# Performance work log

Measured on AMD Instinct MI355X. Metric: run time of the kernel, lower is better.

Reference implementation:

```python
import jax, jax.numpy as jnp
import numpy as np

N = 50000          # total points
C = 256            # channels
H = 8              # heads
D = C // H         # head dim = 32
W = 256            # window size
STRIDE = 128
LENGTHS = [12500, 12500, 12500, 12500]
HID = 512          # ffn hidden = 2.0 * C
EPS = 1e-5


def _build_windows():
    """numpy port of build_windows_1d: returns (M, W) indices and bool mask."""
    idxs, masks = [], []
    start = 0
    for L in LENGTHS:
        n_windows = (L - 1) // STRIDE + 1
        for i in range(n_windows):
            s = i * STRIDE
            b = min(L, s + W)
            cur_len = b - s
            loc = np.arange(s, b, dtype=np.int32) + start
            if W - cur_len > 0:
                loc = np.concatenate([loc, np.full(W - cur_len, loc[-1], dtype=np.int32)])
            m = np.zeros(W, dtype=bool)
            m[:cur_len] = True
            idxs.append(loc)
            masks.append(m)
        start += L
    return np.stack(idxs, 0), np.stack(masks, 0)


def setup_inputs() -> dict:
    key = jax.random.key(0)
    ks = jax.random.split(key, 8)
    def p(k, shape):
        return jax.random.normal(k, shape, dtype=jnp.float32) * 0.02
    win_idx_np, win_mask_np = _build_windows()
    return {
        "x": jax.random.normal(ks[0], (N, C), dtype=jnp.float32),
        "win_idx": jnp.asarray(win_idx_np, dtype=jnp.int32),
        "win_mask": jnp.asarray(win_mask_np),
        "norm1_g": jnp.ones((C,), jnp.float32), "norm1_b": jnp.zeros((C,), jnp.float32),
        "qkv_w": p(ks[1], (C, 3 * C)),
        "proj_w": p(ks[2], (C, C)), "proj_b": jnp.zeros((C,), jnp.float32),
        "ca_norm_g": jnp.ones((C,), jnp.float32), "ca_norm_b": jnp.zeros((C,), jnp.float32),
        "ca_qkv_w": p(ks[3], (C, 3 * C)), "ca_qkv_b": jnp.zeros((3 * C,), jnp.float32),
        "ca_proj_w": p(ks[4], (C, C)), "ca_proj_b": jnp.zeros((C,), jnp.float32),
        "norm2_g": jnp.ones((C,), jnp.float32), "norm2_b": jnp.zeros((C,), jnp.float32),
        "ffn_w1": p(ks[5], (C, HID)), "ffn_b1": jnp.zeros((HID,), jnp.float32),
        "ffn_ln_g": jnp.ones((HID,), jnp.float32), "ffn_ln_b": jnp.zeros((HID,), jnp.float32),
        "ffn_w2": p(ks[6], (HID, C)), "ffn_b2": jnp.zeros((C,), jnp.float32),
    }


def _ln(x, g, b):
    m = jnp.mean(x, axis=-1, keepdims=True)
    v = jnp.mean((x - m) ** 2, axis=-1, keepdims=True)
    return (x - m) * jax.lax.rsqrt(v + EPS) * g + b


def reference(x, win_idx, win_mask,
              norm1_g, norm1_b, qkv_w, proj_w, proj_b,
              ca_norm_g, ca_norm_b, ca_qkv_w, ca_qkv_b, ca_proj_w, ca_proj_b,
              norm2_g, norm2_b, ffn_w1, ffn_b1, ffn_ln_g, ffn_ln_b, ffn_w2, ffn_b2):
    M, Wn = win_idx.shape
    scale = D ** -0.5
    maskf = win_mask[..., None].astype(x.dtype)          # [M, W, 1]

    x_in = _ln(x, norm1_g, norm1_b)                      # [N, C]
    xw = x_in[win_idx]                                   # gather windows [M, W, C]

    # --- Stream A: per-window SDPA ---
    qkv = xw @ qkv_w                                     # [M, W, 3C]
    q, k, v = [t.reshape(M, Wn, H, D).transpose(0, 2, 1, 3)
               for t in jnp.split(qkv, 3, axis=-1)]      # each [M, H, W, D]
    scores = jnp.einsum('mhqd,mhkd->mhqk', q, k) * scale
    scores = jnp.where(win_mask[:, None, None, :], scores, -jnp.inf)
    attn = jax.nn.softmax(scores, axis=-1)
    out = jnp.einsum('mhqk,mhkd->mhqd', attn, v).transpose(0, 2, 1, 3).reshape(M, Wn, C)
    out = (out @ proj_w + proj_b) * maskf                # masked per-window output

    # --- Stream B: centroid attention over M window centroids ---
    wc = jnp.maximum(win_mask.sum(-1, keepdims=True).astype(x.dtype), 1.0)  # [M, 1]
    cent = (xw * maskf).sum(1) / wc                      # [M, C]
    cx = _ln(cent, ca_norm_g, ca_norm_b)
    cqkv = cx @ ca_qkv_w + ca_qkv_b
    cq, ck, cv = [t.reshape(M, H, D).transpose(1, 0, 2)
                  for t in jnp.split(cqkv, 3, axis=-1)]  # each [H, M, D]
    cs = jnp.einsum('hqd,hkd->hqk', cq, ck) * scale
    co = jnp.einsum('hqk,hkd->hqd', jax.nn.softmax(cs, -1), cv)
    co = co.transpose(1, 0, 2).reshape(M, C)
    cent_out = cent + co @ ca_proj_w + ca_proj_b         # residual + proj

    gctx = cent_out[:, None, :] * maskf                  # broadcast global ctx [M, W, C]

    # --- scatter-add back with overlap averaging ---
    total = (out + gctx).reshape(-1, C)
    flat_idx = win_idx.reshape(-1)
    y = jnp.zeros_like(x).at[flat_idx].add(total)
    counts = jnp.zeros((x.shape[0], 1), x.dtype).at[flat_idx].add(
        win_mask.reshape(-1, 1).astype(x.dtype))
    x_out = x + y / jnp.maximum(counts, 1.0)

    # --- FFN (LayerNorm variant) ---
    h1 = _ln(x_out, norm2_g, norm2_b) @ ffn_w1 + ffn_b1
    h1 = jax.nn.relu(_ln(h1, ffn_ln_g, ffn_ln_b))
    return x_out + h1 @ ffn_w2 + ffn_b2
```

## Files before the change

kernel.cpp:

```cpp
#include <hip/hip_runtime.h>

typedef unsigned short ushort;
typedef unsigned int uint;
typedef __attribute__((ext_vector_type(4))) float f32x4;
typedef __attribute__((ext_vector_type(16))) float f32x16;
typedef __attribute__((ext_vector_type(8))) short bf16x8;
typedef __attribute__((ext_vector_type(4))) uint uint32x4;
typedef __attribute__((ext_vector_type(2))) uint uint2v;

#define NPTS 50000
#define C 256
#define CH3 768
#define H 8
#define D 32
#define WW 256
#define HID 512
#define EPSV 1e-5f
#define QK_SCALE 0.17677669529663687f
#define LOG2E 1.4426950408889634f
#define SC_LOG2 (QK_SCALE * LOG2E)

#define BM 128
#define BN 128
#define BK 64
#define NGEMM_QKV 2346
#define NCENT 392
#define NATT 3136
#define NPROJ 1568

#if __has_builtin(__builtin_amdgcn_exp2f)
#define EXP2R(x) __builtin_amdgcn_exp2f(x)
#else
#define EXP2R(x) exp2f(x)
#endif

__device__ inline float bf2f(ushort u) { uint i = ((uint)u) << 16; float f; __builtin_memcpy(&f, &i, 4); return f; }
__device__ inline float bflo(uint u) { uint i = u << 16; float f; __builtin_memcpy(&f, &i, 4); return f; }
__device__ inline float bfhi(uint u) { uint i = u & 0xffff0000u; float f; __builtin_memcpy(&f, &i, 4); return f; }
__device__ inline ushort f2bf(float f) {
  uint i; __builtin_memcpy(&i, &f, 4);
  uint r = i + 0x7fffu + ((i >> 16) & 1u);
  return (ushort)(r >> 16);
}
__device__ inline uint pk2bf(float a, float b) { return (uint)f2bf(a) | ((uint)f2bf(b) << 16); }

__device__ __forceinline__ void gload16(const ushort* g, const ushort* l) {
  __builtin_amdgcn_global_load_lds(
      (const __attribute__((address_space(1))) unsigned int*)(unsigned long long)g,
      (__attribute__((address_space(3))) unsigned int*)(unsigned int)(unsigned long long)l,
      16, 0, 0);
}

__device__ __forceinline__ int xcd_swz(int orig, int nwg) {
  int q8 = nwg >> 3, r8 = nwg & 7;
  int xcd = orig & 7, sub = orig >> 3;
  return (xcd < r8 ? xcd * (q8 + 1) : r8 * (q8 + 1) + (xcd - r8) * q8) + sub;
}

#define BLOCK_REDUCE_2(sv, s2v)                                            \
  {                                                                        \
    _Pragma("unroll")                                                      \
    for (int o_ = 1; o_ < 64; o_ <<= 1) {                                  \
      sv  += __shfl_xor(sv, o_);                                           \
      s2v += __shfl_xor(s2v, o_);                                          \
    }                                                                      \
    __shared__ float ls_[4], ls2_[4];                                      \
    int wid_ = threadIdx.x >> 6;                                           \
    if ((threadIdx.x & 63) == 0) { ls_[wid_] = sv; ls2_[wid_] = s2v; }     \
    __syncthreads();                                                       \
    sv  = ls_[0] + ls_[1] + ls_[2] + ls_[3];                               \
    s2v = ls2_[0] + ls2_[1] + ls2_[2] + ls2_[3];                           \
  }

template <int EPI>
__device__ __forceinline__ void gemm_body(ushort* SMEM, int bid,
                                          const ushort* __restrict__ A,
                                          const ushort* __restrict__ Bt,
                                          void* __restrict__ outp,
                                          const float* __restrict__ bias,
                                          int Mrows, int Ncols, int K) {
  ushort* As = SMEM;
  ushort* Bs = SMEM + BM * BK;
  int t = threadIdx.x;
  int nbn = Ncols >> 7;
  int bm = bid / nbn, bn = bid - bm * nbn;
  int l = t & 63, wv = t >> 6;
  int wr = wv >> 1, wcid = wv & 1;
  int l15 = l & 15, l4 = l >> 4;
  int lr = l >> 3;
  int csrc = ((l & 7) ^ lr) << 3;
  f32x4 acc[4][4];
#pragma unroll
  for (int i = 0; i < 4; ++i)
#pragma unroll
    for (int j = 0; j < 4; ++j) acc[i][j] = (f32x4){0.f, 0.f, 0.f, 0.f};

  int nks = K >> 6;
  for (int ks = 0; ks < nks; ++ks) {
    if (ks) __syncthreads();
#pragma unroll
    for (int i = 0; i < 4; ++i) {
      int rloc = wv * 8 + lr + i * 32;
      int growA = min(bm * BM + rloc, Mrows - 1);
      gload16(&A[(size_t)growA * K + (ks << 6) + csrc], &As[(wv * 8 + i * 32) * BK]);
      gload16(&Bt[(size_t)(bn * BN + rloc) * K + (ks << 6) + csrc], &Bs[(wv * 8 + i * 32) * BK]);
    }
    __syncthreads();
#pragma unroll
    for (int kk = 0; kk < 2; ++kk) {
      bf16x8 af[4], bfr[4];
#pragma unroll
      for (int i = 0; i < 4; ++i) {
        int ra = wr * 64 + i * 16 + l15;
        int ca = (l4 + kk * 4) ^ (ra & 7);
        af[i] = *(const bf16x8*)&As[ra * BK + (ca << 3)];
        int rb = wcid * 64 + i * 16 + l15;
        int cb = (l4 + kk * 4) ^ (rb & 7);
        bfr[i] = *(const bf16x8*)&Bs[rb * BK + (cb << 3)];
      }
      __builtin_amdgcn_s_setprio(1);
#pragma unroll
      for (int i = 0; i < 4; ++i)
#pragma unroll
        for (int j = 0; j < 4; ++j)
          acc[i][j] = __builtin_amdgcn_mfma_f32_16x16x32_bf16(af[i], bfr[j], acc[i][j], 0, 0, 0);
      __builtin_amdgcn_s_setprio(0);
    }
  }

  const int CS = 136;
  ushort* Cs = SMEM;
#pragma unroll
  for (int pass = 0; pass < 2; ++pass) {
    __syncthreads();
    if (wr == pass) {
#pragma unroll
      for (int i = 0; i < 4; ++i)
#pragma unroll
        for (int j = 0; j < 4; ++j)
#pragma unroll
          for (int r = 0; r < 4; ++r) {
            int rl = i * 16 + l4 * 4 + r;
            int cl = wcid * 64 + j * 16 + l15;
            float v = acc[i][j][r];
            if (EPI >= 1) v += bias[bn * BN + cl];
            Cs[rl * CS + cl] = f2bf(v);
          }
    }
    __syncthreads();
    int rl = t >> 2;
    int cq = (t & 3) * 32;
    int grow = bm * BM + pass * 64 + rl;
    if (grow < Mrows) {
      if (EPI <= 1) {
        ushort* orow = (ushort*)outp + (size_t)grow * Ncols + bn * BN + cq;
#pragma unroll
        for (int s = 0; s < 4; ++s)
          *(uint4*)(orow + s * 8) = *(const uint4*)&Cs[rl * CS + cq + s * 8];
      } else {
        float* orow = (float*)outp + (size_t)grow * Ncols + bn * BN + cq;
#pragma unroll
        for (int s = 0; s < 8; ++s) {
          float4 ov = *(float4*)(orow + s * 4);
          const ushort* cp = &Cs[rl * CS + cq + s * 4];
          ov.x += bf2f(cp[0]); ov.y += bf2f(cp[1]);
          ov.z += bf2f(cp[2]); ov.w += bf2f(cp[3]);
          *(float4*)(orow + s * 4) = ov;
        }
      }
    }
  }
}

template <int EPI>
__global__ __launch_bounds__(256, 4) void gemm_bf16(
    const ushort* __restrict__ A, const ushort* __restrict__ Bt, void* __restrict__ outp,
    const float* __restrict__ bias, int Mrows, int Ncols, int K) {
  __shared__ ushort SMEM[(BM + BN) * BK];
  int bid = xcd_swz(blockIdx.x, gridDim.x);
  gemm_body<EPI>(SMEM, bid, A, Bt, outp, bias, Mrows, Ncols, K);
}

__global__ __launch_bounds__(256) void pre_kernel(
    const float* __restrict__ qkv_w, const float* __restrict__ proj_w,
    const float* __restrict__ w1, const float* __restrict__ w2,
    ushort* __restrict__ qkv_wt, ushort* __restrict__ proj_wt,
    ushort* __restrict__ w1t, ushort* __restrict__ w2t,
    const float* __restrict__ x, const float* __restrict__ g, const float* __restrict__ b,
    ushort* __restrict__ xout) {
  int bid = blockIdx.x;
  if (bid < 128) {
    __shared__ float tile[64][65];
    const float* w; ushort* wt; int K, N, boff; float scale; int n_hi;
    if (bid < 48)      { w = qkv_w;  wt = qkv_wt;  K = C;   N = CH3; boff = 0;  scale = SC_LOG2; n_hi = C; }
    else if (bid < 64) { w = proj_w; wt = proj_wt; K = C;   N = C;   boff = 48; scale = 1.f; n_hi = 0; }
    else if (bid < 96) { w = w1;     wt = w1t;     K = C;   N = HID; boff = 64; scale = 1.f; n_hi = 0; }
    else               { w = w2;     wt = w2t;     K = HID; N = C;   boff = 96; scale = 1.f; n_hi = 0; }
    int lb = bid - boff;
    int nbn = N >> 6;
    int bk = lb / nbn, bn = lb - bk * nbn;
    int c = threadIdx.x & 63, r4 = threadIdx.x >> 6;
#pragma unroll
    for (int rr = 0; rr < 16; ++rr) {
      int r = rr * 4 + r4;
      tile[r][c] = w[(size_t)(bk * 64 + r) * N + bn * 64 + c];
    }
    __syncthreads();
#pragma unroll
    for (int rr = 0; rr < 16; ++rr) {
      int r = rr * 4 + r4;
      int n = bn * 64 + r;
      float s = (n < n_hi) ? scale : 1.f;
      wt[(size_t)n * K + bk * 64 + c] = f2bf(tile[c][r] * s);
    }
  } else {
    int wv = threadIdx.x >> 6, lane = threadIdx.x & 63;
    int row = (bid - 128) * 4 + wv;
    float4 v = ((const float4*)(x + (size_t)row * C))[lane];
    float s = v.x + v.y + v.z + v.w;
    float s2 = v.x * v.x + v.y * v.y + v.z * v.z + v.w * v.w;
#pragma unroll
    for (int o = 1; o < 64; o <<= 1) { s += __shfl_xor(s, o); s2 += __shfl_xor(s2, o); }
    float mean = s * (1.0f / C);
    float var = s2 * (1.0f / C) - mean * mean;
    float rs = rsqrtf(var + EPSV);
    float4 gv = ((const float4*)g)[lane];
    float4 bv = ((const float4*)b)[lane];
    uint2 pk;
    pk.x = pk2bf((v.x - mean) * rs * gv.x + bv.x, (v.y - mean) * rs * gv.y + bv.y);
    pk.y = pk2bf((v.z - mean) * rs * gv.z + bv.z, (v.w - mean) * rs * gv.w + bv.w);
    ((uint2*)(xout + (size_t)row * C))[lane] = pk;
  }
}

__global__ __launch_bounds__(256, 4) void qkv_cent_kernel(
    const ushort* __restrict__ xb, const int* __restrict__ win_idx,
    const float* __restrict__ lng, const float* __restrict__ lnb,
    const float* __restrict__ caw, const float* __restrict__ cab,
    float* __restrict__ cent, float* __restrict__ cqkv, float* __restrict__ kT,
    int* __restrict__ wc_i, const ushort* __restrict__ qkv_wt, ushort* __restrict__ qkvb, int M) {
  __shared__ ushort SMEM[(BM + BN) * BK];
  int bid = blockIdx.x;
  if (bid < NCENT) {
    float* fbase = (float*)SMEM;
    float (*red)[257] = (float(*)[257])fbase;
    float* cxl = fbase + 8 * 257;
    int m = bid, t = threadIdx.x;
    int i0 = win_idx[m * WW];
    int iL = win_idx[m * WW + WW - 1];
    int wc = iL - i0 + 1;
    if (t == 0) wc_i[m] = wc;
    int rg = t >> 5, cg = t & 31;
    float acc[8] = {0.f, 0.f, 0.f, 0.f, 0.f, 0.f, 0.f, 0.f};
    for (int r = rg; r < wc; r += 8) {
      uint4 u = *(const uint4*)(xb + (size_t)(i0 + r) * C + cg * 8);
      acc[0] += bflo(u.x); acc[1] += bfhi(u.x);
      acc[2] += bflo(u.y); acc[3] += bfhi(u.y);
      acc[4] += bflo(u.z); acc[5] += bfhi(u.z);
      acc[6] += bflo(u.w); acc[7] += bfhi(u.w);
    }
#pragma unroll
    for (int j = 0; j < 8; ++j) red[rg][cg * 8 + j] = acc[j];
    __syncthreads();
    float sum = red[0][t];
#pragma unroll
    for (int k = 1; k < 8; ++k) sum += red[k][t];
    float cv = sum / (float)wc;
    cent[m * C + t] = cv;
    float s = cv, s2 = cv * cv;
    BLOCK_REDUCE_2(s, s2);
    float mean = s * (1.0f / C);
    float var = s2 * (1.0f / C) - mean * mean;
    float rs = rsqrtf(var + EPSV);
    cxl[t] = (cv - mean) * rs * lng[t] + lnb[t];
    __syncthreads();
    for (int j = t; j < CH3; j += 256) {
      float a = cab[j];
      for (int c2 = 0; c2 < C; ++c2) a += cxl[c2] * caw[(size_t)c2 * CH3 + j];
      cqkv[(size_t)m * CH3 + j] = a;
      if (j >= C && j < 2 * C) kT[(size_t)(j - C) * M + m] = a;
    }
  } else {
    int g = xcd_swz(bid - NCENT, NGEMM_QKV);
    gemm_body<0>(SMEM, g, xb, qkv_wt, qkvb, nullptr, NPTS, CH3, C);
  }
}

__global__ __launch_bounds__(256) void attn_cent_kernel(
    const ushort* __restrict__ qkv, const int* __restrict__ win_idx,
    const int* __restrict__ wc_i, ushort* __restrict__ ao,
    const float* __restrict__ cqkv, const float* __restrict__ kT,
    float* __restrict__ co, int* __restrict__ slots, int M) {
  __shared__ char SM[37376];
  int bid = blockIdx.x;
  int t = threadIdx.x;
  int lane = t & 63;
  int l31 = lane & 31, hp = lane >> 5;

  if (bid < NCENT) {
    float (*p_lds)[400] = (float(*)[400])(float*)SM;
    int wv = t >> 6;
    int mq = bid;
#pragma unroll
    for (int pp = 0; pp < 2; ++pp) {
      int h = wv * 2 + pp;
      const float* qp = cqkv + (size_t)mq * CH3 + h * D;
      float q[D];
#pragma unroll
      for (int d = 0; d < D; ++d) q[d] = qp[d] * SC_LOG2;
      float s[7];
      float mi = -3.0e38f;
#pragma unroll
      for (int j = 0; j < 7; ++j) {
        int mk = lane + 64 * j;
        s[j] = -3.0e38f;
        if (mk < M) {
          float a = 0.f;
#pragma unroll
          for (int d = 0; d < D; ++d) a += q[d] * kT[(size_t)(h * D + d) * M + mk];
          s[j] = a;
          mi = fmaxf(mi, a);
        }
      }
#pragma unroll
      for (int off = 1; off < 64; off <<= 1) mi = fmaxf(mi, __shfl_xor(mi, off));
      float li = 0.f;
#pragma unroll
      for (int j = 0; j < 7; ++j) {
        int mk = lane + 64 * j;
        if (mk < M) { float pv = EXP2R(s[j] - mi); li += pv; p_lds[h][mk] = pv; }
      }
#pragma unroll
      for (int off = 1; off < 64; off <<= 1) li += __shfl_xor(li, off);
      int d = l31, hpp = hp;
      const int HALF = 196;
      int k0 = hpp * HALF;
      const float* vbase = cqkv + 2 * C + h * D + d;
      float o0 = 0.f, o1 = 0.f, o2 = 0.f, o3 = 0.f;
      for (int kk = 0; kk < HALF / 4; ++kk) {
        int k = k0 + kk * 4;
        o0 += p_lds[h][k + 0] * vbase[(size_t)(k + 0) * CH3];
        o1 += p_lds[h][k + 1] * vbase[(size_t)(k + 1) * CH3];
        o2 += p_lds[h][k + 2] * vbase[(size_t)(k + 2) * CH3];
        o3 += p_lds[h][k + 3] * vbase[(size_t)(k + 3) * CH3];
      }
      float o = (o0 + o1) + (o2 + o3);
      o += __shfl_xor(o, 32);
      if (lane < 32) co[(size_t)mq * C + h * D + d] = o / li;
    }
    return;
  }
  if (bid < 2 * NCENT) {
    int m = bid - NCENT;
    int wc = wc_i[m];
    int i0 = win_idx[m * WW];
    if (t < wc) slots[2 * (i0 + t) + (t >= 128 ? 0 : 1)] = m * WW + t;
    return;
  }

  ushort* K_lds = (ushort*)SM;
  uint* Vt = (uint*)(SM + 20480);
  int abid = xcd_swz(bid - 2 * NCENT, NATT);
  int m = abid >> 3, h = abid & 7;
  int wcv = wc_i[m];
  int i0 = win_idx[m * WW];
  int wq = t >> 6;

  bf16x8 qf[2][2];
#pragma unroll
  for (int qb = 0; qb < 2; ++qb) {
    int qrow = i0 + min(wq * 64 + qb * 32 + l31, wcv - 1);
#pragma unroll
    for (int c = 0; c < 2; ++c)
      qf[qb][c] = *(const bf16x8*)(qkv + (size_t)qrow * CH3 + h * D + c * 16 + hp * 8);
  }

  if (t >= 128) {
    int base = (t - 128) * 2;
#pragma unroll
    for (int rr = 0; rr < 2; ++rr) {
      int row = base + rr;
      const uint4* src = (const uint4*)(qkv + (size_t)(i0 + min(row, wcv - 1)) * CH3 + C + h * D);
      *(uint4*)&K_lds[row * 40 + 0]  = src[0];
      *(uint4*)&K_lds[row * 40 + 8]  = src[1];
      *(uint4*)&K_lds[row * 40 + 16] = src[2];
      *(uint4*)&K_lds[row * 40 + 24] = src[3];
    }
  } else {
    int k0 = t * 2;
    const uint* s0 = (const uint*)(qkv + (size_t)(i0 + min(k0, wcv - 1)) * CH3 + 2 * C + h * D);
    const uint* s1 = (const uint*)(qkv + (size_t)(i0 + min(k0 + 1, wcv - 1)) * CH3 + 2 * C + h * D);
#pragma unroll
    for (int w2 = 0; w2 < 16; ++w2) {
      uint a = s0[w2], b = s1[w2];
      Vt[(2 * w2) * 132 + t] = (a & 0xffffu) | (b << 16);
      Vt[(2 * w2 + 1) * 132 + t] = (a >> 16) | (b & 0xffff0000u);
    }
  }
  __syncthreads();

  const f32x16 zv = {0.f, 0.f, 0.f, 0.f, 0.f, 0.f, 0.f, 0.f,
                     0.f, 0.f, 0.f, 0.f, 0.f, 0.f, 0.f, 0.f};
  f32x16 O0 = zv, O1 = zv;
  float l0 = 0.f, l1 = 0.f;

  auto tile = [&](int kt, bool partial) {
    int kbase = kt * 32;
    bf16x8 ka0 = *(const bf16x8*)&K_lds[(kbase + l31) * 40 + hp * 8];
    bf16x8 ka1 = *(const bf16x8*)&K_lds[(kbase + l31) * 40 + 16 + hp * 8];
    uint4 v0raw = *(const uint4*)&Vt[l31 * 132 + kt * 16 + hp * 4];
    uint4 v1raw = *(const uint4*)&Vt[l31 * 132 + kt * 16 + 8 + hp * 4];
    bf16x8 vb0 = __builtin_bit_cast(bf16x8, v0raw);
    bf16x8 vb1 = __builtin_bit_cast(bf16x8, v1raw);

    auto qbody = [&](const bf16x8& q0, const bf16x8& q1, f32x16& O, float& lq) {
      __builtin_amdgcn_s_setprio(1);
      f32x16 st = __builtin_amdgcn_mfma_f32_32x32x16_bf16(ka0, q0, zv, 0, 0, 0);
      st = __builtin_amdgcn_mfma_f32_32x32x16_bf16(ka1, q1, st, 0, 0, 0);
      __builtin_amdgcn_s_setprio(0);
      if (partial) {
        int kb_h = kbase + 4 * hp;
#pragma unroll
        for (int r = 0; r < 16; ++r) {
          int crow = (r & 3) + 8 * (r >> 2);
          st[r] = (kb_h + crow >= wcv) ? -3.0e38f : st[r];
        }
      }
      float ls = 0.f;
#pragma unroll
      for (int r = 0; r < 16; ++r) { st[r] = EXP2R(st[r]); ls += st[r]; }
      lq += ls;
      uint w[8];
#pragma unroll
      for (int i = 0; i < 8; ++i) {
        uint o;
        asm("v_cvt_pk_bf16_f32 %0, %1, %2" : "=v"(o) : "v"(st[2 * i]), "v"(st[2 * i + 1]));
        w[i] = o;
      }
#if __has_builtin(__builtin_amdgcn_permlane32_swap)
      uint2v s02 = __builtin_amdgcn_permlane32_swap(w[0], w[2], false, false);
      uint2v s13 = __builtin_amdgcn_permlane32_swap(w[1], w[3], false, false);
      uint2v s46 = __builtin_amdgcn_permlane32_swap(w[4], w[6], false, false);
      uint2v s57 = __builtin_amdgcn_permlane32_swap(w[5], w[7], false, false);
      uint32x4 pa0u = {s02.x, s13.x, s02.y, s13.y};
      uint32x4 pa1u = {s46.x, s57.x, s46.y, s57.y};
#else
      uint sw0 = __shfl_xor((int)w[0], 32), sw1 = __shfl_xor((int)w[1], 32);
      uint sw2 = __shfl_xor((int)w[2], 32), sw3 = __shfl_xor((int)w[3], 32);
      uint sw4 = __shfl_xor((int)w[4], 32), sw5 = __shfl_xor((int)w[5], 32);
      uint sw6 = __shfl_xor((int)w[6], 32), sw7 = __shfl_xor((int)w[7], 32);
      uint32x4 pa0u = {hp ? sw2 : w[0], hp ? sw3 : w[1], hp ? w[2] : sw0, hp ? w[3] : sw1};
      uint32x4 pa1u = {hp ? sw6 : w[4], hp ? sw7 : w[5], hp ? w[6] : sw4, hp ? w[7] : sw5};
#endif
      bf16x8 pa0 = __builtin_bit_cast(bf16x8, pa0u);
      bf16x8 pa1 = __builtin_bit_cast(bf16x8, pa1u);
      __builtin_amdgcn_s_setprio(1);
      O = __builtin_amdgcn_mfma_f32_32x32x16_bf16(pa0, vb0, O, 0, 0, 0);
      O = __builtin_amdgcn_mfma_f32_32x32x16_bf16(pa1, vb1, O, 0, 0, 0);
      __builtin_amdgcn_s_setprio(0);
    };
    qbody(qf[0][0], qf[0][1], O0, l0);
    qbody(qf[1][0], qf[1][1], O1, l1);
  };

  int fullt = wcv >> 5;
  for (int kt = 0; kt < fullt; ++kt) tile(kt, false);
  if (wcv & 31) tile(fullt, true);

  auto epi = [&](f32x16& O, float lq, int qb) {
    float lt = lq + __shfl_xor(lq, 32);
    float inv = 1.f / lt;
#pragma unroll
    for (int r = 0; r < 16; ++r) {
      int qi = (r & 3) + 8 * (r >> 2) + 4 * hp;
      float iv = __shfl(inv, qi);
      int row = m * WW + wq * 64 + qb * 32 + qi;
      ao[(size_t)row * C + h * D + l31] = f2bf(O[r] * iv);
    }
  };
  epi(O0, l0, 0);
  epi(O1, l1, 1);
}

__global__ __launch_bounds__(256, 4) void proj_cent_kernel(
    const ushort* __restrict__ aob, const ushort* __restrict__ proj_wt,
    ushort* __restrict__ pout, const float* __restrict__ proj_b,
    const float* __restrict__ co, const float* __restrict__ cent,
    const float* __restrict__ pw, const float* __restrict__ pb,
    float* __restrict__ cent_o, int M) {
  __shared__ ushort SMEM[(BM + BN) * BK];
  int bid = blockIdx.x;
  if (bid < NCENT) {
    float* co_lds = (float*)SMEM;
    int mq = bid, t = threadIdx.x;
    co_lds[t] = co[(size_t)mq * C + t];
    __syncthreads();
    float a = pb[t] + cent[(size_t)mq * C + t];
    for (int k = 0; k < C; ++k) a += co_lds[k] * pw[(size_t)k * C + t];
    cent_o[(size_t)mq * C + t] = a;
    return;
  }
  int g = xcd_swz(bid - NCENT, NPROJ);
  gemm_body<1>(SMEM, g, aob, proj_wt, pout, proj_b, M * WW, C, C);
}

__global__ __launch_bounds__(256) void combine_ln_kernel(
    const float* __restrict__ x, const int* __restrict__ slots,
    const ushort* __restrict__ pout, const float* __restrict__ cent_o,
    const float* __restrict__ g, const float* __restrict__ b,
    float* __restrict__ xout, ushort* __restrict__ lnx) {
  int wv = threadIdx.x >> 6, lane = threadIdx.x & 63;
  int i = blockIdx.x * 4 + wv;
  int e0 = slots[2 * i], e1 = slots[2 * i + 1];
  float4 xv = ((const float4*)(x + (size_t)i * C))[lane];
  float a0 = 0.f, a1 = 0.f, a2 = 0.f, a3 = 0.f, cnt = 0.f;
  if (e0 >= 0) {
    uint2 pv = ((const uint2*)(pout + (size_t)e0 * C))[lane];
    float4 cv = ((const float4*)(cent_o + (size_t)(e0 >> 8) * C))[lane];
    a0 += bflo(pv.x) + cv.x; a1 += bfhi(pv.x) + cv.y;
    a2 += bflo(pv.y) + cv.z; a3 += bfhi(pv.y) + cv.w;
    cnt += 1.f;
  }
  if (e1 >= 0) {
    uint2 pv = ((const uint2*)(pout + (size_t)e1 * C))[lane];
    float4 cv = ((const float4*)(cent_o + (size_t)(e1 >> 8) * C))[lane];
    a0 += bflo(pv.x) + cv.x; a1 += bfhi(pv.x) + cv.y;
    a2 += bflo(pv.y) + cv.z; a3 += bfhi(pv.y) + cv.w;
    cnt += 1.f;
  }
  float inv = cnt > 0.f ? 1.f / cnt : 0.f;
  float o0 = xv.x + a0 * inv, o1 = xv.y + a1 * inv;
  float o2 = xv.z + a2 * inv, o3 = xv.w + a3 * inv;
  float s = o0 + o1 + o2 + o3;
  float s2 = o0 * o0 + o1 * o1 + o2 * o2 + o3 * o3;
#pragma unroll
  for (int o = 1; o < 64; o <<= 1) { s += __shfl_xor(s, o); s2 += __shfl_xor(s2, o); }
  float mean = s * (1.0f / C);
  float var = s2 * (1.0f / C) - mean * mean;
  float rs = rsqrtf(var + EPSV);
  ((float4*)(xout + (size_t)i * C))[lane] = make_float4(o0, o1, o2, o3);
  float4 gv = ((const float4*)g)[lane];
  float4 bv = ((const float4*)b)[lane];
  uint2 pk;
  pk.x = pk2bf((o0 - mean) * rs * gv.x + bv.x, (o1 - mean) * rs * gv.y + bv.y);
  pk.y = pk2bf((o2 - mean) * rs * gv.z + bv.z, (o3 - mean) * rs * gv.w + bv.w);
  ((uint2*)(lnx + (size_t)i * C))[lane] = pk;
}

__global__ __launch_bounds__(256) void hln_relu_kernel(ushort* __restrict__ h,
                                                       const float* __restrict__ g,
                                                       const float* __restrict__ b) {
  int wv = threadIdx.x >> 6, lane = threadIdx.x & 63;
  int i = blockIdx.x * 4 + wv;
  uint4 u = ((const uint4*)(h + (size_t)i * HID))[lane];
  float v[8] = {bflo(u.x), bfhi(u.x), bflo(u.y), bfhi(u.y),
                bflo(u.z), bfhi(u.z), bflo(u.w), bfhi(u.w)};
  float s = 0.f, s2 = 0.f;
#pragma unroll
  for (int j = 0; j < 8; ++j) { s += v[j]; s2 += v[j] * v[j]; }
#pragma unroll
  for (int o = 1; o < 64; o <<= 1) { s += __shfl_xor(s, o); s2 += __shfl_xor(s2, o); }
  float mean = s * (1.0f / HID);
  float var = s2 * (1.0f / HID) - mean * mean;
  float rs = rsqrtf(var + EPSV);
  float4 g0 = ((const float4*)g)[lane * 2], g1 = ((const float4*)g)[lane * 2 + 1];
  float4 b0 = ((const float4*)b)[lane * 2], b1 = ((const float4*)b)[lane * 2 + 1];
  float ga[8] = {g0.x, g0.y, g0.z, g0.w, g1.x, g1.y, g1.z, g1.w};
  float ba[8] = {b0.x, b0.y, b0.z, b0.w, b1.x, b1.y, b1.z, b1.w};
  float r[8];
#pragma unroll
  for (int j = 0; j < 8; ++j) r[j] = fmaxf((v[j] - mean) * rs * ga[j] + ba[j], 0.f);
  uint4 outu = make_uint4(pk2bf(r[0], r[1]), pk2bf(r[2], r[3]),
                          pk2bf(r[4], r[5]), pk2bf(r[6], r[7]));
  ((uint4*)(h + (size_t)i * HID))[lane] = outu;
}

extern "C" void kernel_launch(void* const* d_in, const int* in_sizes, int n_in,
                              void* d_out, int out_size, void* d_ws, size_t ws_size,
                              hipStream_t stream) {
  (void)n_in; (void)ws_size; (void)out_size;
  const float* x         = (const float*)d_in[0];
  const int*   win_idx   = (const int*)d_in[1];
  const float* norm1_g   = (const float*)d_in[3];
  const float* norm1_b   = (const float*)d_in[4];
  const float* qkv_w     = (const float*)d_in[5];
  const float* proj_w    = (const float*)d_in[6];
  const float* proj_b    = (const float*)d_in[7];
  const float* ca_norm_g = (const float*)d_in[8];
  const float* ca_norm_b = (const float*)d_in[9];
  const float* ca_qkv_w  = (const float*)d_in[10];
  const float* ca_qkv_b  = (const float*)d_in[11];
  const float* ca_proj_w = (const float*)d_in[12];
  const float* ca_proj_b = (const float*)d_in[13];
  const float* norm2_g   = (const float*)d_in[14];
  const float* norm2_b   = (const float*)d_in[15];
  const float* ffn_w1    = (const float*)d_in[16];
  const float* ffn_b1    = (const float*)d_in[17];
  const float* ffn_ln_g  = (const float*)d_in[18];
  const float* ffn_ln_b  = (const float*)d_in[19];
  const float* ffn_w2    = (const float*)d_in[20];
  const float* ffn_b2    = (const float*)d_in[21];

  const int M = in_sizes[1] / WW;

  char* p = (char*)d_ws;
  auto alloc = [&](size_t bytes) { char* r = p; p += (bytes + 255) & ~(size_t)255; return r; };
  ushort* x_in_b = (ushort*)alloc((size_t)NPTS * C * 2);
  ushort* qkvb   = (ushort*)alloc((size_t)NPTS * CH3 * 2);
  ushort* aob    = (ushort*)alloc((size_t)M * WW * C * 2);
  ushort* pout   = (ushort*)alloc((size_t)M * WW * C * 2);
  int*   slots   = (int*)  alloc((size_t)NPTS * 2 * 4);
  int*   wc_i    = (int*)  alloc((size_t)M * 4);
  float* cent    = (float*)alloc((size_t)M * C * 4);
  float* cqkv    = (float*)alloc((size_t)M * CH3 * 4);
  float* kT      = (float*)alloc((size_t)C * M * 4);
  float* co      = (float*)alloc((size_t)M * C * 4);
  float* cent_o  = (float*)alloc((size_t)M * C * 4);
  ushort* qkv_wt = (ushort*)alloc((size_t)CH3 * C * 2);
  ushort* proj_wt= (ushort*)alloc((size_t)C * C * 2);
  ushort* w1t    = (ushort*)alloc((size_t)HID * C * 2);
  ushort* w2t    = (ushort*)alloc((size_t)C * HID * 2);
  float* yout    = (float*)d_out;

  hipMemsetAsync(slots, 0xFF, (size_t)NPTS * 2 * 4, stream);

  pre_kernel<<<128 + NPTS / 4, 256, 0, stream>>>(
      qkv_w, proj_w, ffn_w1, ffn_w2, qkv_wt, proj_wt, w1t, w2t,
      x, norm1_g, norm1_b, x_in_b);

  qkv_cent_kernel<<<NCENT + NGEMM_QKV, 256, 0, stream>>>(
      x_in_b, win_idx, ca_norm_g, ca_norm_b, ca_qkv_w, ca_qkv_b,
      cent, cqkv, kT, wc_i, qkv_wt, qkvb, M);

  attn_cent_kernel<<<2 * NCENT + NATT, 256, 0, stream>>>(
      qkvb, win_idx, wc_i, aob, cqkv, kT, co, slots, M);

  proj_cent_kernel<<<NCENT + NPROJ, 256, 0, stream>>>(
      aob, proj_wt, pout, proj_b, co, cent, ca_proj_w, ca_proj_b, cent_o, M);

  ushort* lnx = x_in_b;
  combine_ln_kernel<<<NPTS / 4, 256, 0, stream>>>(x, slots, pout, cent_o, norm2_g, norm2_b,
                                                  yout, lnx);
  ushort* h1 = qkvb;
  const int gm = (NPTS + BM - 1) / BM;
  gemm_bf16<1><<<gm * (HID / BN), 256, 0, stream>>>(lnx, w1t, h1, ffn_b1,
                                                    NPTS, HID, C);
  hln_relu_kernel<<<NPTS / 4, 256, 0, stream>>>(h1, ffn_ln_g, ffn_ln_b);
  gemm_bf16<2><<<gm * (C / BN), 256, 0, stream>>>(h1, w2t, yout, ffn_b2,
                                                  NPTS, C, HID);
}
```

Before: 356.4 us.

## Move centroid QKV projection from scalar loops to a bf16 MFMA GEMM

The per-window centroid LayerNorm output is now written as bf16, and the centroid QKV projection runs as a separate MFMA GEMM kernel with a new epilogue that writes fp32 cqkv plus the transposed K. Previously each centroid block computed 768 outputs with a serial 256-long fp32 dot product over global weights. The ca_qkv weights are transposed to bf16 in the pre-kernel. This adds an extra launch, lowers precision on the centroid path to bf16, and uses an uncoalesced kT write in the epilogue.

```diff
diff --git a/kernel.cpp b/kernel.cpp
--- a/kernel.cpp
+++ b/kernel.cpp
@@ -78,7 +78,9 @@
                                           const ushort* __restrict__ Bt,
                                           void* __restrict__ outp,
                                           const float* __restrict__ bias,
-                                          int Mrows, int Ncols, int K) {
+                                          int Mrows, int Ncols, int K,
+                                          float* __restrict__ kTout = nullptr,
+                                          int Mtot = 0) {
   ushort* As = SMEM;
   ushort* Bs = SMEM + BM * BK;
   int t = threadIdx.x;
@@ -128,6 +130,24 @@
     }
   }
 
+  if (EPI == 3) {
+#pragma unroll
+    for (int i = 0; i < 4; ++i)
+#pragma unroll
+      for (int j = 0; j < 4; ++j)
+#pragma unroll
+        for (int r = 0; r < 4; ++r) {
+          int row = bm * BM + wr * 64 + i * 16 + l4 * 4 + r;
+          int col = bn * BN + wcid * 64 + j * 16 + l15;
+          if (row < Mrows) {
+            float v = acc[i][j][r] + bias[col];
+            ((float*)outp)[(size_t)row * Ncols + col] = v;
+            if (col >= C && col < 2 * C) kTout[(size_t)(col - C) * Mtot + row] = v;
+          }
+        }
+    return;
+  }
+
   const int CS = 136;
   ushort* Cs = SMEM;
 #pragma unroll
@@ -181,21 +201,32 @@
   gemm_body<EPI>(SMEM, bid, A, Bt, outp, bias, Mrows, Ncols, K);
 }
 
+__global__ __launch_bounds__(256, 4) void caqkv_gemm_kernel(
+    const ushort* __restrict__ cxb, const ushort* __restrict__ caqkv_wt,
+    float* __restrict__ cqkv, const float* __restrict__ bias,
+    float* __restrict__ kT, int M) {
+  __shared__ ushort SMEM[(BM + BN) * BK];
+  gemm_body<3>(SMEM, blockIdx.x, cxb, caqkv_wt, cqkv, bias, M, CH3, C, kT, M);
+}
+
 __global__ __launch_bounds__(256) void pre_kernel(
     const float* __restrict__ qkv_w, const float* __restrict__ proj_w,
     const float* __restrict__ w1, const float* __restrict__ w2,
+    const float* __restrict__ caqkv_w,
     ushort* __restrict__ qkv_wt, ushort* __restrict__ proj_wt,
     ushort* __restrict__ w1t, ushort* __restrict__ w2t,
+    ushort* __restrict__ caqkv_wt,
     const float* __restrict__ x, const float* __restrict__ g, const float* __restrict__ b,
     ushort* __restrict__ xout) {
   int bid = blockIdx.x;
-  if (bid < 128) {
+  if (bid < 176) {
     __shared__ float tile[64][65];
     const float* w; ushort* wt; int K, N, boff; float scale; int n_hi;
-    if (bid < 48)      { w = qkv_w;  wt = qkv_wt;  K = C;   N = CH3; boff = 0;  scale = SC_LOG2; n_hi = C; }
-    else if (bid < 64) { w = proj_w; wt = proj_wt; K = C;   N = C;   boff = 48; scale = 1.f; n_hi = 0; }
-    else if (bid < 96) { w = w1;     wt = w1t;     K = C;   N = HID; boff = 64; scale = 1.f; n_hi = 0; }
-    else               { w = w2;     wt = w2t;     K = HID; N = C;   boff = 96; scale = 1.f; n_hi = 0; }
+    if (bid < 48)       { w = qkv_w;   wt = qkv_wt;   K = C;   N = CH3; boff = 0;   scale = SC_LOG2; n_hi = C; }
+    else if (bid < 64)  { w = proj_w;  wt = proj_wt;  K = C;   N = C;   boff = 48;  scale = 1.f; n_hi = 0; }
+    else if (bid < 96)  { w = w1;      wt = w1t;      K = C;   N = HID; boff = 64;  scale = 1.f; n_hi = 0; }
+    else if (bid < 128) { w = w2;      wt = w2t;      K = HID; N = C;   boff = 96;  scale = 1.f; n_hi = 0; }
+    else                { w = caqkv_w; wt = caqkv_wt; K = C;   N = CH3; boff = 128; scale = 1.f; n_hi = 0; }
     int lb = bid - boff;
     int nbn = N >> 6;
     int bk = lb / nbn, bn = lb - bk * nbn;
@@ -215,7 +246,7 @@
     }
   } else {
     int wv = threadIdx.x >> 6, lane = threadIdx.x & 63;
-    int row = (bid - 128) * 4 + wv;
+    int row = (bid - 176) * 4 + wv;
     float4 v = ((const float4*)(x + (size_t)row * C))[lane];
     float s = v.x + v.y + v.z + v.w;
     float s2 = v.x * v.x + v.y * v.y + v.z * v.z + v.w * v.w;
@@ -236,15 +267,12 @@
 __global__ __launch_bounds__(256, 4) void qkv_cent_kernel(
     const ushort* __restrict__ xb, const int* __restrict__ win_idx,
     const float* __restrict__ lng, const float* __restrict__ lnb,
-    const float* __restrict__ caw, const float* __restrict__ cab,
-    float* __restrict__ cent, float* __restrict__ cqkv, float* __restrict__ kT,
+    float* __restrict__ cent, ushort* __restrict__ cxb,
     int* __restrict__ wc_i, const ushort* __restrict__ qkv_wt, ushort* __restrict__ qkvb, int M) {
   __shared__ ushort SMEM[(BM + BN) * BK];
   int bid = blockIdx.x;
   if (bid < NCENT) {
-    float* fbase = (float*)SMEM;
-    float (*red)[257] = (float(*)[257])fbase;
-    float* cxl = fbase + 8 * 257;
+    float (*red)[257] = (float(*)[257])(float*)SMEM;
     int m = bid, t = threadIdx.x;
     int i0 = win_idx[m * WW];
     int iL = win_idx[m * WW + WW - 1];
@@ -272,14 +300,7 @@
     float mean = s * (1.0f / C);
     float var = s2 * (1.0f / C) - mean * mean;
     float rs = rsqrtf(var + EPSV);
-    cxl[t] = (cv - mean) * rs * lng[t] + lnb[t];
-    __syncthreads();
-    for (int j = t; j < CH3; j += 256) {
-      float a = cab[j];
-      for (int c2 = 0; c2 < C; ++c2) a += cxl[c2] * caw[(size_t)c2 * CH3 + j];
-      cqkv[(size_t)m * CH3 + j] = a;
-      if (j >= C && j < 2 * C) kT[(size_t)(j - C) * M + m] = a;
-    }
+    cxb[(size_t)m * C + t] = f2bf((cv - mean) * rs * lng[t] + lnb[t]);
   } else {
     int g = xcd_swz(bid - NCENT, NGEMM_QKV);
     gemm_body<0>(SMEM, g, xb, qkv_wt, qkvb, nullptr, NPTS, CH3, C);
@@ -612,6 +633,7 @@
   int*   slots   = (int*)  alloc((size_t)NPTS * 2 * 4);
   int*   wc_i    = (int*)  alloc((size_t)M * 4);
   float* cent    = (float*)alloc((size_t)M * C * 4);
+  ushort* cxb    = (ushort*)alloc((size_t)M * C * 2);
   float* cqkv    = (float*)alloc((size_t)M * CH3 * 4);
   float* kT      = (float*)alloc((size_t)C * M * 4);
   float* co      = (float*)alloc((size_t)M * C * 4);
@@ -620,17 +642,21 @@
   ushort* proj_wt= (ushort*)alloc((size_t)C * C * 2);
   ushort* w1t    = (ushort*)alloc((size_t)HID * C * 2);
   ushort* w2t    = (ushort*)alloc((size_t)C * HID * 2);
+  ushort* caqkv_wt = (ushort*)alloc((size_t)CH3 * C * 2);
   float* yout    = (float*)d_out;
 
   hipMemsetAsync(slots, 0xFF, (size_t)NPTS * 2 * 4, stream);
 
-  pre_kernel<<<128 + NPTS / 4, 256, 0, stream>>>(
-      qkv_w, proj_w, ffn_w1, ffn_w2, qkv_wt, proj_wt, w1t, w2t,
+  pre_kernel<<<176 + NPTS / 4, 256, 0, stream>>>(
+      qkv_w, proj_w, ffn_w1, ffn_w2, ca_qkv_w,
+      qkv_wt, proj_wt, w1t, w2t, caqkv_wt,
       x, norm1_g, norm1_b, x_in_b);
 
   qkv_cent_kernel<<<NCENT + NGEMM_QKV, 256, 0, stream>>>(
-      x_in_b, win_idx, ca_norm_g, ca_norm_b, ca_qkv_w, ca_qkv_b,
-      cent, cqkv, kT, wc_i, qkv_wt, qkvb, M);
+      x_in_b, win_idx, ca_norm_g, ca_norm_b, cent, cxb, wc_i, qkv_wt, qkvb, M);
+
+  caqkv_gemm_kernel<<<((M + BM - 1) / BM) * (CH3 / BN), 256, 0, stream>>>(
+      cxb, caqkv_wt, cqkv, ca_qkv_b, kT, M);
 
   attn_cent_kernel<<<2 * NCENT + NATT, 256, 0, stream>>>(
       qkvb, win_idx, wc_i, aob, cqkv, kT, co, slots, M);
```

Measured after the change: 358.2 us. No clear change (+0.5%).
